# Performance work log

Measured on AMD Instinct MI355X. Metric: run time of the kernel, lower is better.

## Reference

```python
import jax, jax.numpy as jnp
import numpy as np

D, U, H = 3, 256, 8
DH = U // H
B, N, E = 128, 128, 512
BN_SCALE = 1.0 / np.sqrt(1.0 + 1e-3)  # keras BatchNorm inference with init moving stats (mean=0, var=1)


def setup_inputs() -> dict:
    key = jax.random.key(0)
    k = jax.random.split(key, 16)
    p = lambda kk, sh: jax.random.normal(kk, sh, jnp.float32) * 0.05
    return {
        "node_attr": jax.random.normal(k[0], (B, N, U), jnp.float32),
        "edge_attr": jax.random.normal(k[1], (B, E, U), jnp.float32),
        "edge_indices": jax.random.randint(k[2], (B, E, 2), 0, N, dtype=jnp.int32),
        "W_edge": p(k[3], (D, 3 * U, U)), "b_edge": jnp.zeros((D, U)),
        "gamma_e": jnp.ones((D, U)), "beta_e": jnp.zeros((D, U)),
        "W_node": p(k[4], (D, U, U)), "b_node": jnp.zeros((D, U)),
        "gamma_n": jnp.ones((D, U)), "beta_n": jnp.zeros((D, U)),
        "W_gat": p(k[5], (D, U, H, DH)), "a_gat": p(k[6], (D, H, 2 * DH + U)), "b_gat": jnp.zeros((D, H)),
        "W_gru": p(k[7], (D, U, 3 * U)), "U_gru": p(k[8], (D, U, 3 * U)), "b_gru": jnp.zeros((D, 3 * U)),
        "W_p1": p(k[9], (U, U)), "b_p1": jnp.zeros((U,)),
        "W_p2": p(k[10], (U, U // 2)), "b_p2": jnp.zeros((U // 2,)),
    }


def _bn(x, gamma, beta):
    # inference batchnorm with moving_mean=0, moving_var=1
    return x * (gamma * BN_SCALE) + beta


def _gather(nodes, idx):
    # nodes [B,N,F], idx [B,E] -> [B,E,F]
    return jnp.take_along_axis(nodes, idx[..., None], axis=1)


def _gat_one(h, eidx, edge, a, b):
    # h [N,H,DH], eidx [E,2], edge [E,U]; aggregate messages from src (col 1) at tgt (col 0)
    tgt, src = eidx[:, 0], eidx[:, 1]
    hi, hj = h[tgt], h[src]
    logit = (jnp.einsum('ehd,hd->eh', hi, a[:, :DH])
             + jnp.einsum('ehd,hd->eh', hj, a[:, DH:2 * DH])
             + edge @ a[:, 2 * DH:].T + b)
    logit = jax.nn.leaky_relu(logit, 0.2)
    # per-target-node segment softmax over variable-degree neighborhoods
    m = jnp.full((N, H), -1e9, logit.dtype).at[tgt].max(logit)
    ex = jnp.exp(logit - m[tgt])
    den = jnp.zeros((N, H), logit.dtype).at[tgt].add(ex) + 1e-9
    att = ex / den[tgt]
    out = jnp.zeros((N, H, DH), h.dtype).at[tgt].add(att[..., None] * hj)
    return out.reshape(N, H * DH)


def reference(node_attr, edge_attr, edge_indices, W_edge, b_edge, gamma_e, beta_e,
              W_node, b_node, gamma_n, beta_n, W_gat, a_gat, b_gat,
              W_gru, U_gru, b_gru, W_p1, b_p1, W_p2, b_p2):
    nodes, edges = node_attr, edge_attr
    tgt_idx = edge_indices[..., 0]
    src_idx = edge_indices[..., 1]
    for d in range(D):
        # edge update: gather endpoints, concat with edge feats, MLP, graph batchnorm
        e_in = _gather(nodes, src_idx)   # GatherNodesOutgoing
        e_out = _gather(nodes, tgt_idx)  # GatherNodesIngoing
        ec = jnp.concatenate([e_in, e_out, edges], axis=-1)  # [B,E,3U]
        e_up = _bn(jax.nn.relu(ec @ W_edge[d] + b_edge[d]), gamma_e[d], beta_e[d])
        # multi-head GAT attention over edges
        h = jnp.einsum('bnf,fhd->bnhd', nodes, W_gat[d])
        attended = jax.nn.relu(jax.vmap(_gat_one, in_axes=(0, 0, 0, None, None))(
            h, edge_indices, e_up, a_gat[d], b_gat[d]))
        # node MLP + batchnorm
        n_up = _bn(jax.nn.relu(nodes @ W_node[d] + b_node[d]), gamma_n[d], beta_n[d])
        # GRU update: state = n_up, input = attended
        xp = attended @ W_gru[d] + b_gru[d]
        hp = n_up @ U_gru[d]
        z = jax.nn.sigmoid(xp[..., :U] + hp[..., :U])
        r = jax.nn.sigmoid(xp[..., U:2 * U] + hp[..., U:2 * U])
        hh = jnp.tanh(xp[..., 2 * U:] + r * hp[..., 2 * U:])
        nodes = z * n_up + (1.0 - z) * hh
        edges = e_up
    emb = jnp.mean(nodes, axis=1)
    emb = jax.nn.relu(emb @ W_p1 + b_p1)
    emb = jax.nn.relu(emb @ W_p2 + b_p2)
    # inference-mode view augmentation is identity, so both views equal the base embedding
    views = jnp.stack([emb, emb], axis=1)  # [B, num_views, U//2]
    return emb, views
```

## Files before the change

### kernel.cpp

```cpp
#include <hip/hip_runtime.h>
#include <hip/hip_bf16.h>

constexpr int Dn  = 3;
constexpr int Un  = 256;
constexpr int Hn  = 8;
constexpr int DHn = 32;
constexpr int Bn  = 128;
constexpr int Nn  = 128;
constexpr int En  = 512;
constexpr float BN_SCALE_C = 0.9995003746877732f;

#define LB __launch_bounds__(256)
#define LB8 __launch_bounds__(512)

typedef short bf16x8 __attribute__((ext_vector_type(8)));
typedef unsigned short u16x8 __attribute__((ext_vector_type(8)));
typedef float f32x4 __attribute__((ext_vector_type(4)));
#define MFMA16(a, b, c) __builtin_amdgcn_mfma_f32_16x16x32_bf16(a, b, c, 0, 0, 0)

__device__ __forceinline__ void gload16(const void* g, void* l) {
  __builtin_amdgcn_global_load_lds(
      (const __attribute__((address_space(1))) void*)g,
      (__attribute__((address_space(3))) void*)l, 16, 0, 0);
}
__device__ __forceinline__ float sigm(float x) { return 1.f / (1.f + expf(-x)); }
__device__ __forceinline__ float bf2f(unsigned short u) {
  return __uint_as_float((unsigned)u << 16);
}

__global__ LB void k_f2bf(const float* __restrict__ in,
                          __hip_bfloat16* __restrict__ out, int n) {
  int i = (blockIdx.x * 256 + threadIdx.x) * 4;
  if (i + 3 < n) {
    float4 v = *reinterpret_cast<const float4*>(in + i);
    out[i + 0] = __float2bfloat16(v.x);
    out[i + 1] = __float2bfloat16(v.y);
    out[i + 2] = __float2bfloat16(v.z);
    out[i + 3] = __float2bfloat16(v.w);
  }
}

__global__ LB void k_prep_edge(const float* __restrict__ W,
                               __hip_bfloat16* __restrict__ Wt) {
  int idx = blockIdx.x * 256 + threadIdx.x;
  int d = idx / (Un * 3 * Un);
  int rem = idx % (Un * 3 * Un);
  int n = rem / (3 * Un);
  int k = rem % (3 * Un);
  Wt[idx] = __float2bfloat16(W[(size_t)d * 3 * Un * Un + (size_t)k * Un + n]);
}

__global__ LB void k_prep_hn(const float* __restrict__ Wg,
                             const float* __restrict__ Wn,
                             __hip_bfloat16* __restrict__ Wt) {
  int idx = blockIdx.x * 256 + threadIdx.x;
  int d = idx / (512 * 256);
  int rem = idx % (512 * 256);
  int n = rem / 256;
  int k = rem % 256;
  float v = (n < 256) ? Wg[(size_t)d * 65536 + k * 256 + n]
                      : Wn[(size_t)d * 65536 + k * 256 + (n - 256)];
  Wt[idx] = __float2bfloat16(v);
}

__global__ LB void k_prep_gru2(const float* __restrict__ W,
                               const float* __restrict__ U,
                               __hip_bfloat16* __restrict__ Wt) {
  int idx = blockIdx.x * 256 + threadIdx.x;
  int d = idx / (768 * 512);
  int rem = idx % (768 * 512);
  int j2 = rem >> 9;
  int k = rem & 511;
  const size_t wb = (size_t)d * 196608;
  float v = (k < 256) ? W[wb + k * 768 + j2] : U[wb + (k - 256) * 768 + j2];
  Wt[idx] = __float2bfloat16(v);
}

__global__ LB8 void k_edge_mfma(const __hip_bfloat16* __restrict__ nodes,
                                const __hip_bfloat16* __restrict__ edges,
                                const int* __restrict__ eidx,
                                const __hip_bfloat16* __restrict__ Wt,
                                const float* __restrict__ bias,
                                const float* __restrict__ gamma,
                                const float* __restrict__ beta,
                                __hip_bfloat16* __restrict__ e_up) {
  __shared__ __align__(16) short As[128 * 64];
  __shared__ __align__(16) short Bs[256 * 64];
  const int tid = threadIdx.x, lane = tid & 63;
  const int w = tid >> 6, wr = w >> 2, wc = w & 3;
  const int bid = blockIdx.x;
  const int wgid = (bid & 7) * 64 + (bid >> 3);
  const int row0 = wgid * 128;
  const __hip_bfloat16 *pa0[2], *pa1[2], *pa2[2], *pb[4];
  int sxa[2], sxb[4];
#pragma unroll
  for (int i = 0; i < 2; ++i) {
    int c = i * 512 + tid, row = c >> 3, slot = c & 7;
    int R = row0 + row, b = R >> 9, e = R & 511;
    int tt = eidx[(b * En + e) * 2 + 0];
    int ss = eidx[(b * En + e) * 2 + 1];
    pa0[i] = nodes + (size_t)(b * Nn + ss) * Un;
    pa1[i] = nodes + (size_t)(b * Nn + tt) * Un;
    pa2[i] = edges + (size_t)(b * En + e) * Un;
    sxa[i] = (slot ^ (row & 7)) * 8;
  }
#pragma unroll
  for (int i = 0; i < 4; ++i) {
    int c = i * 512 + tid, j = c >> 3, slot = c & 7;
    pb[i] = Wt + (size_t)j * 768;
    sxb[i] = (slot ^ (j & 7)) * 8;
  }
  f32x4 acc[4][4] = {};
  const int ldsb = (tid & 448) * 16;
  for (int kt = 0; kt < 768; kt += 64) {
    const int region = kt >> 8, koff = kt & 255;
#pragma unroll
    for (int i = 0; i < 2; ++i) {
      const __hip_bfloat16* s = (region == 0) ? pa0[i] : (region == 1 ? pa1[i] : pa2[i]);
      gload16(s + koff + sxa[i], (char*)As + i * 8192 + ldsb);
    }
#pragma unroll
    for (int i = 0; i < 4; ++i)
      gload16(pb[i] + kt + sxb[i], (char*)Bs + i * 8192 + ldsb);
    __syncthreads();
#pragma unroll
    for (int ks = 0; ks < 2; ++ks) {
      const int lc = ks * 4 + (lane >> 4);
      bf16x8 af[4], bfv[4];
#pragma unroll
      for (int mi = 0; mi < 4; ++mi) {
        int row = wr * 64 + mi * 16 + (lane & 15);
        af[mi] = *(const bf16x8*)((const char*)As + row * 128 + ((lc ^ (row & 7)) << 4));
      }
#pragma unroll
      for (int ni = 0; ni < 4; ++ni) {
        int col = wc * 64 + ni * 16 + (lane & 15);
        bfv[ni] = *(const bf16x8*)((const char*)Bs + col * 128 + ((lc ^ (col & 7)) << 4));
      }
#pragma unroll
      for (int mi = 0; mi < 4; ++mi)
#pragma unroll
        for (int ni = 0; ni < 4; ++ni)
          acc[mi][ni] = MFMA16(af[mi], bfv[ni], acc[mi][ni]);
    }
    __syncthreads();
  }
#pragma unroll
  for (int mi = 0; mi < 4; ++mi)
#pragma unroll
    for (int ni = 0; ni < 4; ++ni) {
      int C = wc * 64 + ni * 16 + (lane & 15);
      float gs = gamma[C] * BN_SCALE_C, bt = beta[C], bi = bias[C];
#pragma unroll
      for (int r = 0; r < 4; ++r) {
        int R = row0 + wr * 64 + mi * 16 + (lane >> 4) * 4 + r;
        float v = acc[mi][ni][r] + bi;
        v = fmaxf(v, 0.f) * gs + bt;
        e_up[(size_t)R * Un + C] = __float2bfloat16(v);
      }
    }
}

__global__ LB8 void k_hn_mfma(const __hip_bfloat16* __restrict__ A,
                              const __hip_bfloat16* __restrict__ Wt,
                              const float* __restrict__ nb,
                              const float* __restrict__ ng,
                              const float* __restrict__ nbe,
                              __hip_bfloat16* __restrict__ h_bf,
                              __hip_bfloat16* __restrict__ nupb) {
  __shared__ __align__(16) short As[128 * 64];
  __shared__ __align__(16) short Bs[256 * 64];
  const int tid = threadIdx.x, lane = tid & 63;
  const int w = tid >> 6, wr = w >> 2, wc = w & 3;
  const int bid = blockIdx.x;
  const int wgid = (bid & 7) * 32 + (bid >> 3);
  const int row0 = (wgid >> 1) * 128, col0 = (wgid & 1) * 256;
  const __hip_bfloat16 *pa[2], *pb[4];
  int sxa[2], sxb[4];
#pragma unroll
  for (int i = 0; i < 2; ++i) {
    int c = i * 512 + tid, row = c >> 3, slot = c & 7;
    pa[i] = A + (size_t)(row0 + row) * Un;
    sxa[i] = (slot ^ (row & 7)) * 8;
  }
#pragma unroll
  for (int i = 0; i < 4; ++i) {
    int c = i * 512 + tid, j = c >> 3, slot = c & 7;
    pb[i] = Wt + (size_t)(col0 + j) * Un;
    sxb[i] = (slot ^ (j & 7)) * 8;
  }
  f32x4 acc[4][4] = {};
  const int ldsb = (tid & 448) * 16;
  for (int kt = 0; kt < 256; kt += 64) {
#pragma unroll
    for (int i = 0; i < 2; ++i)
      gload16(pa[i] + kt + sxa[i], (char*)As + i * 8192 + ldsb);
#pragma unroll
    for (int i = 0; i < 4; ++i)
      gload16(pb[i] + kt + sxb[i], (char*)Bs + i * 8192 + ldsb);
    __syncthreads();
#pragma unroll
    for (int ks = 0; ks < 2; ++ks) {
      const int lc = ks * 4 + (lane >> 4);
      bf16x8 af[4], bfv[4];
#pragma unroll
      for (int mi = 0; mi < 4; ++mi) {
        int row = wr * 64 + mi * 16 + (lane & 15);
        af[mi] = *(const bf16x8*)((const char*)As + row * 128 + ((lc ^ (row & 7)) << 4));
      }
#pragma unroll
      for (int ni = 0; ni < 4; ++ni) {
        int col = wc * 64 + ni * 16 + (lane & 15);
        bfv[ni] = *(const bf16x8*)((const char*)Bs + col * 128 + ((lc ^ (col & 7)) << 4));
      }
#pragma unroll
      for (int mi = 0; mi < 4; ++mi)
#pragma unroll
        for (int ni = 0; ni < 4; ++ni)
          acc[mi][ni] = MFMA16(af[mi], bfv[ni], acc[mi][ni]);
    }
    __syncthreads();
  }
  const bool is_h = (col0 < 256);
#pragma unroll
  for (int mi = 0; mi < 4; ++mi)
#pragma unroll
    for (int ni = 0; ni < 4; ++ni) {
      int c2 = wc * 64 + ni * 16 + (lane & 15);
#pragma unroll
      for (int r = 0; r < 4; ++r) {
        int R = row0 + wr * 64 + mi * 16 + (lane >> 4) * 4 + r;
        float v = acc[mi][ni][r];
        if (is_h) {
          h_bf[(size_t)R * Un + c2] = __float2bfloat16(v);
        } else {
          v += nb[c2];
          v = fmaxf(v, 0.f) * (ng[c2] * BN_SCALE_C) + nbe[c2];
          nupb[(size_t)R * Un + c2] = __float2bfloat16(v);
        }
      }
    }
}

__global__ LB void k_gru_mfma2(const __hip_bfloat16* __restrict__ attb,
                               const __hip_bfloat16* __restrict__ nupb,
                               const __hip_bfloat16* __restrict__ Wt,
                               const float* __restrict__ bg,
                               __hip_bfloat16* __restrict__ nodes_out) {
  __shared__ __align__(16) short As[128 * 64];
  __shared__ __align__(16) short Bs[96 * 64];
  const int tid = threadIdx.x, lane = tid & 63;
  const int w = tid >> 6, wr = w >> 1, wc = w & 1;
  const int bid = blockIdx.x;
  const int wgid = (bid & 7) * 128 + (bid >> 3);
  const int row0 = (wgid >> 3) * 128, c0 = (wgid & 7) * 32;
  const __hip_bfloat16 *paA[4], *paN[4], *pb[3];
  int sxa[4], sxb[3];
#pragma unroll
  for (int i = 0; i < 4; ++i) {
    int c = i * 256 + tid, row = c >> 3, slot = c & 7;
    paA[i] = attb + (size_t)(row0 + row) * Un;
    paN[i] = nupb + (size_t)(row0 + row) * Un;
    sxa[i] = (slot ^ (row & 7)) * 8;
  }
#pragma unroll
  for (int i = 0; i < 3; ++i) {
    int l = i * 256 + tid, j = l >> 3, slot = l & 7;
    int grow = (j < 32) ? (c0 + j) : (j < 64) ? (256 + c0 + (j - 32))
                                              : (512 + c0 + (j - 64));
    pb[i] = Wt + (size_t)grow * 512;
    sxb[i] = (slot ^ (j & 7)) * 8;
  }
  f32x4 acc[4][4] = {};
  const int ldsb = (tid & 192) * 16;
  for (int kt = 0; kt < 512; kt += 64) {
    const int koff = kt & 255;
    const bool rA = kt < 256;
#pragma unroll
    for (int i = 0; i < 4; ++i) {
      const __hip_bfloat16* s = rA ? paA[i] : paN[i];
      gload16(s + koff + sxa[i], (char*)As + i * 4096 + ldsb);
    }
#pragma unroll
    for (int i = 0; i < 3; ++i)
      gload16(pb[i] + kt + sxb[i], (char*)Bs + i * 4096 + ldsb);
    __syncthreads();
    const int g2 = rA ? 2 : 3;
#pragma unroll
    for (int ks = 0; ks < 2; ++ks) {
      const int lc = ks * 4 + (lane >> 4);
      bf16x8 af[4], bv[3];
      const int jj = wc * 16 + (lane & 15);
      const int jsw = (lc ^ (jj & 7)) << 4;
      bv[0] = *(const bf16x8*)((const char*)Bs + jj * 128 + jsw);
      bv[1] = *(const bf16x8*)((const char*)Bs + (32 + jj) * 128 + jsw);
      bv[2] = *(const bf16x8*)((const char*)Bs + (64 + jj) * 128 + jsw);
#pragma unroll
      for (int mi = 0; mi < 4; ++mi) {
        int row = wr * 64 + mi * 16 + (lane & 15);
        af[mi] = *(const bf16x8*)((const char*)As + row * 128 + ((lc ^ (row & 7)) << 4));
      }
#pragma unroll
      for (int mi = 0; mi < 4; ++mi) {
        acc[0][mi] = MFMA16(af[mi], bv[0], acc[0][mi]);
        acc[1][mi] = MFMA16(af[mi], bv[1], acc[1][mi]);
        acc[g2][mi] = MFMA16(af[mi], bv[2], acc[g2][mi]);
      }
    }
    __syncthreads();
  }
  {
    const int c = c0 + wc * 16 + (lane & 15);
    const float bz = bg[c], br = bg[256 + c], bh = bg[512 + c];
    const unsigned short* nu_u = (const unsigned short*)nupb;
#pragma unroll
    for (int mi = 0; mi < 4; ++mi)
#pragma unroll
      for (int r = 0; r < 4; ++r) {
        int R = row0 + wr * 64 + mi * 16 + (lane >> 4) * 4 + r;
        float z  = sigm(acc[0][mi][r] + bz);
        float rr = sigm(acc[1][mi][r] + br);
        float hh = tanhf(acc[2][mi][r] + bh + rr * acc[3][mi][r]);
        float nu = bf2f(nu_u[(size_t)R * Un + c]);
        nodes_out[(size_t)R * Un + c] = __float2bfloat16(z * nu + (1.f - z) * hh);
      }
  }
}

__global__ LB void k_elog_mfma(const __hip_bfloat16* __restrict__ e_up,
                               const float* __restrict__ a_gat,
                               float* __restrict__ elog) {
  __shared__ __align__(16) short at[16 * 264];
  const int tid = threadIdx.x, lane = tid & 63, w = tid >> 6;
  for (int l = tid; l < 16 * 264; l += 256) {
    int col = l / 264, k = l % 264;
    float v = (col < 8 && k < 256) ? a_gat[col * 320 + 64 + k] : 0.f;
    __hip_bfloat16 b = __float2bfloat16(v);
    at[l] = *reinterpret_cast<short*>(&b);
  }
  __syncthreads();
  const int rowbase = blockIdx.x * 256 + w * 64;
  const int lrow = lane & 15, lk = (lane >> 4) * 8;
  f32x4 acc[4] = {};
#pragma unroll
  for (int kt = 0; kt < 256; kt += 32) {
    bf16x8 bf = *(const bf16x8*)(at + lrow * 264 + kt + lk);
#pragma unroll
    for (int mi = 0; mi < 4; ++mi) {
      bf16x8 af = *(const bf16x8*)(e_up + (size_t)(rowbase + mi * 16 + lrow) * 256 + kt + lk);
      acc[mi] = MFMA16(af, bf, acc[mi]);
    }
  }
  if (lrow < 8) {
#pragma unroll
    for (int mi = 0; mi < 4; ++mi)
#pragma unroll
      for (int r = 0; r < 4; ++r) {
        int row = rowbase + mi * 16 + (lane >> 4) * 4 + r;
        elog[(size_t)row * 8 + lrow] = acc[mi][r];
      }
  }
}

__global__ LB void k_gat3(const __hip_bfloat16* __restrict__ h,
                          const float* __restrict__ elog,
                          const int* __restrict__ eidx,
                          const float* __restrict__ a_gat,
                          const float* __restrict__ b_gat,
                          __hip_bfloat16* __restrict__ att_bf) {
  const int b = blockIdx.x, hg = blockIdx.y;
  __shared__ int s_tgt[En], s_src[En];
  __shared__ float s_at[4][32], s_as[4][32];
  __shared__ float s_lt[Nn][4], s_ls[Nn][4];
  __shared__ float s_L[En][4];
  __shared__ int s_cnt[Nn], s_start[Nn], s_cur[Nn];
  __shared__ short s_ord[En];
  __shared__ float s_bg[4];
  __shared__ __align__(16) unsigned short hl[Nn][136];
  const int tid = threadIdx.x;
  if (tid < 4) s_bg[tid] = b_gat[hg * 4 + tid];
  if (tid < 128) {
    int q = tid >> 5, d = tid & 31;
    s_at[q][d] = a_gat[(hg * 4 + q) * 320 + d];
    s_as[q][d] = a_gat[(hg * 4 + q) * 320 + 32 + d];
  }
  for (int e = tid; e < En; e += 256) {
    s_tgt[e] = eidx[(b * En + e) * 2 + 0];
    s_src[e] = eidx[(b * En + e) * 2 + 1];
  }
  for (int l = tid; l < Nn; l += 256) s_cnt[l] = 0;
  for (int l = tid; l < En * 4; l += 256) {
    int e = l >> 2, q = l & 3;
    s_L[e][q] = elog[(size_t)(b * En + e) * 8 + hg * 4 + q];
  }
  const unsigned short* hu = (const unsigned short*)h;
  for (int l = tid; l < Nn * 16; l += 256) {
    int row = l >> 4, c8 = l & 15;
    u16x8 v = *(const u16x8*)(hu + (size_t)(b * Nn + row) * Un + hg * 128 + c8 * 8);
    *(u16x8*)&hl[row][c8 * 8] = v;
  }
  __syncthreads();
  for (int p = tid; p < Nn * 4; p += 256) {
    int n = p >> 2, q = p & 3;
    const unsigned short* hr = &hl[n][q * 32];
    float lt = 0.f, ls = 0.f;
#pragma unroll
    for (int c8 = 0; c8 < 4; ++c8) {
      u16x8 v = *(const u16x8*)(hr + c8 * 8);
#pragma unroll
      for (int j = 0; j < 8; ++j) {
        float f = bf2f(v[j]);
        int d = c8 * 8 + j;
        lt += f * s_at[q][d];
        ls += f * s_as[q][d];
      }
    }
    s_lt[n][q] = lt; s_ls[n][q] = ls;
  }
  for (int e = tid; e < En; e += 256) atomicAdd(&s_cnt[s_tgt[e]], 1);
  __syncthreads();
  if (tid == 0) {
    int acc = 0;
    for (int n = 0; n < Nn; ++n) { s_start[n] = acc; s_cur[n] = acc; acc += s_cnt[n]; }
  }
  __syncthreads();
  for (int e = tid; e < En; e += 256) {
    int pos = atomicAdd(&s_cur[s_tgt[e]], 1);
    s_ord[pos] = (short)e;
  }
  for (int l = tid; l < En * 4; l += 256) {
    int e = l >> 2, q = l & 3;
    float v = s_lt[s_tgt[e]][q] + s_ls[s_src[e]][q] + s_L[e][q] + s_bg[q];
    v = (v > 0.f) ? v : 0.2f * v;
    s_L[e][q] = v;
  }
  __syncthreads();
  for (int p = tid; p < Nn * 4; p += 256) {
    const int n = p >> 2, q = p & 3;
    const int st = s_start[n], cn = s_cnt[n];
    float m = -1e9f;
    for (int i = 0; i < cn; ++i) m = fmaxf(m, s_L[s_ord[st + i]][q]);
    float den = 1e-9f;
    for (int i = 0; i < cn; ++i) {
      const int e = s_ord[st + i];
      float ex = expf(s_L[e][q] - m);
      s_L[e][q] = ex;
      den += ex;
    }
    const float inv = 1.f / den;
    float acc[32] = {};
    for (int i = 0; i < cn; ++i) {
      const int e = s_ord[st + i];
      const float wgt = s_L[e][q] * inv;
      const unsigned short* hs = &hl[s_src[e]][q * 32];
#pragma unroll
      for (int c8 = 0; c8 < 4; ++c8) {
        u16x8 v = *(const u16x8*)(hs + c8 * 8);
#pragma unroll
        for (int j = 0; j < 8; ++j) acc[c8 * 8 + j] += wgt * bf2f(v[j]);
      }
    }
    __hip_bfloat16* ob = att_bf + (size_t)(b * Nn + n) * Un + (hg * 4 + q) * DHn;
#pragma unroll
    for (int d = 0; d < 32; ++d) ob[d] = __float2bfloat16(fmaxf(acc[d], 0.f));
  }
}

__global__ LB void k_pool(const __hip_bfloat16* __restrict__ nodes,
                          const float* __restrict__ Wp1, const float* __restrict__ bp1,
                          const float* __restrict__ Wp2, const float* __restrict__ bp2,
                          float* __restrict__ out) {
  const int b = blockIdx.x, tid = threadIdx.x;
  __shared__ float e0[256], e1[256];
  float s = 0.f;
  for (int n = 0; n < Nn; ++n) s += __bfloat162float(nodes[(size_t)(b * Nn + n) * Un + tid]);
  e0[tid] = s * (1.f / Nn);
  __syncthreads();
  float a1 = bp1[tid];
  for (int k = 0; k < 256; ++k) a1 += e0[k] * Wp1[k * 256 + tid];
  e1[tid] = fmaxf(a1, 0.f);
  __syncthreads();
  if (tid < 128) {
    float a2 = bp2[tid];
    for (int k = 0; k < 256; ++k) a2 += e1[k] * Wp2[k * 128 + tid];
    a2 = fmaxf(a2, 0.f);
    out[b * 128 + tid] = a2;
    out[Bn * 128 + b * 256 + tid] = a2;
    out[Bn * 128 + b * 256 + 128 + tid] = a2;
  }
}

extern "C" void kernel_launch(void* const* d_in, const int* in_sizes, int n_in,
                              void* d_out, int out_size, void* d_ws, size_t ws_size,
                              hipStream_t stream) {
  const float* node_attr = (const float*)d_in[0];
  const float* edge_attr = (const float*)d_in[1];
  const int*   eidx      = (const int*)d_in[2];
  const float* W_edge    = (const float*)d_in[3];
  const float* b_edge    = (const float*)d_in[4];
  const float* gamma_e   = (const float*)d_in[5];
  const float* beta_e    = (const float*)d_in[6];
  const float* W_node    = (const float*)d_in[7];
  const float* b_node    = (const float*)d_in[8];
  const float* gamma_n   = (const float*)d_in[9];
  const float* beta_n    = (const float*)d_in[10];
  const float* W_gat     = (const float*)d_in[11];
  const float* a_gat     = (const float*)d_in[12];
  const float* b_gat     = (const float*)d_in[13];
  const float* W_gru     = (const float*)d_in[14];
  const float* U_gru     = (const float*)d_in[15];
  const float* b_gru     = (const float*)d_in[16];
  const float* W_p1      = (const float*)d_in[17];
  const float* b_p1      = (const float*)d_in[18];
  const float* W_p2      = (const float*)d_in[19];
  const float* b_p2      = (const float*)d_in[20];

  char* p = (char*)d_ws;
  auto alloc = [&](size_t bytes) { char* q = p; p += (bytes + 255) & ~255ull; return q; };
  const size_t NODE_EL = (size_t)Bn * Nn * Un;
  const size_t EDGE_EL = (size_t)Bn * En * Un;
  __hip_bfloat16* nodes_bf = (__hip_bfloat16*)alloc(NODE_EL * 2);
  __hip_bfloat16* h_bf   = (__hip_bfloat16*)alloc(NODE_EL * 2);
  __hip_bfloat16* nup_bf = (__hip_bfloat16*)alloc(NODE_EL * 2);
  __hip_bfloat16* att_bf = (__hip_bfloat16*)alloc(NODE_EL * 2);
  float* elog   = (float*)alloc((size_t)Bn * En * 8 * 4);
  __hip_bfloat16* edges_a = (__hip_bfloat16*)alloc(EDGE_EL * 2);
  __hip_bfloat16* edges_b = (__hip_bfloat16*)alloc(EDGE_EL * 2);
  __hip_bfloat16* Wt_e   = (__hip_bfloat16*)alloc((size_t)Dn * 256 * 768 * 2);
  __hip_bfloat16* Wt_hn  = (__hip_bfloat16*)alloc((size_t)Dn * 512 * 256 * 2);
  __hip_bfloat16* Wt_gru = (__hip_bfloat16*)alloc((size_t)Dn * 768 * 512 * 2);

  k_f2bf<<<(int)(EDGE_EL / 1024), 256, 0, stream>>>(edge_attr, edges_a, (int)EDGE_EL);
  k_f2bf<<<(int)(NODE_EL / 1024), 256, 0, stream>>>(node_attr, nodes_bf, (int)NODE_EL);
  k_prep_edge<<<(Dn * 256 * 768) / 256, 256, 0, stream>>>(W_edge, Wt_e);
  k_prep_hn<<<(Dn * 512 * 256) / 256, 256, 0, stream>>>(W_gat, W_node, Wt_hn);
  k_prep_gru2<<<(Dn * 768 * 512) / 256, 256, 0, stream>>>(W_gru, U_gru, Wt_gru);

  __hip_bfloat16* ein = edges_a;
  __hip_bfloat16* eout = edges_b;
  for (int d = 0; d < Dn; ++d) {
    k_edge_mfma<<<512, 512, 0, stream>>>(
        nodes_bf, ein, eidx, Wt_e + (size_t)d * 256 * 768, b_edge + d * Un,
        gamma_e + d * Un, beta_e + d * Un, eout);
    k_hn_mfma<<<256, 512, 0, stream>>>(
        nodes_bf, Wt_hn + (size_t)d * 512 * 256, b_node + d * Un,
        gamma_n + d * Un, beta_n + d * Un, h_bf, nup_bf);
    k_elog_mfma<<<(Bn * En) / 256, 256, 0, stream>>>(
        eout, a_gat + (size_t)d * Hn * 320, elog);
    k_gat3<<<dim3(Bn, 2), 256, 0, stream>>>(
        h_bf, elog, eidx, a_gat + (size_t)d * Hn * 320, b_gat + d * Hn, att_bf);
    k_gru_mfma2<<<1024, 256, 0, stream>>>(
        att_bf, nup_bf, Wt_gru + (size_t)d * 768 * 512, b_gru + d * 3 * Un,
        nodes_bf);
    __hip_bfloat16* t = ein; ein = eout; eout = t;
  }
  k_pool<<<Bn, 256, 0, stream>>>(nodes_bf, W_p1, b_p1, W_p2, b_p2, (float*)d_out);
}
```

Before: 369.4 us.

## Split GAT kernel per head and widen GRU GEMM tile to 512 threads

The GAT aggregation kernel now launches one block per (batch, head) instead of per (batch, 4-head group), giving 4x more blocks. It also splits the weighted-sum accumulation across two threads per node, using 16 accumulators each instead of 32. The GRU GEMM moves to 512-thread blocks covering 64 output columns per gate instead of 32, halving the grid and reusing each A tile across more columns. The trade-off is more redundant index/count setup per GAT block and higher per-block LDS and register pressure in the GRU kernel.

```diff
diff --git a/kernel.cpp b/kernel.cpp
--- a/kernel.cpp
+++ b/kernel.cpp
@@ -242,59 +242,58 @@
     }
 }
 
-__global__ LB void k_gru_mfma2(const __hip_bfloat16* __restrict__ attb,
-                               const __hip_bfloat16* __restrict__ nupb,
-                               const __hip_bfloat16* __restrict__ Wt,
-                               const float* __restrict__ bg,
-                               __hip_bfloat16* __restrict__ nodes_out) {
+__global__ LB8 void k_gru_mfma3(const __hip_bfloat16* __restrict__ attb,
+                                const __hip_bfloat16* __restrict__ nupb,
+                                const __hip_bfloat16* __restrict__ Wt,
+                                const float* __restrict__ bg,
+                                __hip_bfloat16* __restrict__ nodes_out) {
   __shared__ __align__(16) short As[128 * 64];
-  __shared__ __align__(16) short Bs[96 * 64];
+  __shared__ __align__(16) short Bs[192 * 64];
   const int tid = threadIdx.x, lane = tid & 63;
-  const int w = tid >> 6, wr = w >> 1, wc = w & 1;
+  const int w = tid >> 6, wr = w >> 2, wc = w & 3;
   const int bid = blockIdx.x;
-  const int wgid = (bid & 7) * 128 + (bid >> 3);
-  const int row0 = (wgid >> 3) * 128, c0 = (wgid & 7) * 32;
-  const __hip_bfloat16 *paA[4], *paN[4], *pb[3];
-  int sxa[4], sxb[3];
-#pragma unroll
-  for (int i = 0; i < 4; ++i) {
-    int c = i * 256 + tid, row = c >> 3, slot = c & 7;
+  const int wgid = (bid & 7) * 64 + (bid >> 3);
+  const int row0 = (wgid >> 2) * 128, c0 = (wgid & 3) * 64;
+  const __hip_bfloat16 *paA[2], *paN[2], *pb[3];
+  int sxa[2], sxb[3];
+#pragma unroll
+  for (int i = 0; i < 2; ++i) {
+    int c = i * 512 + tid, row = c >> 3, slot = c & 7;
     paA[i] = attb + (size_t)(row0 + row) * Un;
     paN[i] = nupb + (size_t)(row0 + row) * Un;
     sxa[i] = (slot ^ (row & 7)) * 8;
   }
 #pragma unroll
   for (int i = 0; i < 3; ++i) {
-    int l = i * 256 + tid, j = l >> 3, slot = l & 7;
-    int grow = (j < 32) ? (c0 + j) : (j < 64) ? (256 + c0 + (j - 32))
-                                              : (512 + c0 + (j - 64));
-    pb[i] = Wt + (size_t)grow * 512;
+    int l = i * 512 + tid, j = l >> 3, slot = l & 7;
+    int sec = j >> 6, jj = j & 63;
+    pb[i] = Wt + (size_t)(sec * 256 + c0 + jj) * 512;
     sxb[i] = (slot ^ (j & 7)) * 8;
   }
   f32x4 acc[4][4] = {};
-  const int ldsb = (tid & 192) * 16;
+  const int ldsb = (tid & 448) * 16;
   for (int kt = 0; kt < 512; kt += 64) {
     const int koff = kt & 255;
     const bool rA = kt < 256;
 #pragma unroll
-    for (int i = 0; i < 4; ++i) {
+    for (int i = 0; i < 2; ++i) {
       const __hip_bfloat16* s = rA ? paA[i] : paN[i];
-      gload16(s + koff + sxa[i], (char*)As + i * 4096 + ldsb);
+      gload16(s + koff + sxa[i], (char*)As + i * 8192 + ldsb);
     }
 #pragma unroll
     for (int i = 0; i < 3; ++i)
-      gload16(pb[i] + kt + sxb[i], (char*)Bs + i * 4096 + ldsb);
+      gload16(pb[i] + kt + sxb[i], (char*)Bs + i * 8192 + ldsb);
     __syncthreads();
     const int g2 = rA ? 2 : 3;
 #pragma unroll
     for (int ks = 0; ks < 2; ++ks) {
       const int lc = ks * 4 + (lane >> 4);
       bf16x8 af[4], bv[3];
-      const int jj = wc * 16 + (lane & 15);
-      const int jsw = (lc ^ (jj & 7)) << 4;
-      bv[0] = *(const bf16x8*)((const char*)Bs + jj * 128 + jsw);
-      bv[1] = *(const bf16x8*)((const char*)Bs + (32 + jj) * 128 + jsw);
-      bv[2] = *(const bf16x8*)((const char*)Bs + (64 + jj) * 128 + jsw);
+#pragma unroll
+      for (int s = 0; s < 3; ++s) {
+        int j = s * 64 + wc * 16 + (lane & 15);
+        bv[s] = *(const bf16x8*)((const char*)Bs + j * 128 + ((lc ^ (j & 7)) << 4));
+      }
 #pragma unroll
       for (int mi = 0; mi < 4; ++mi) {
         int row = wr * 64 + mi * 16 + (lane & 15);
@@ -362,47 +361,42 @@
   }
 }
 
-__global__ LB void k_gat3(const __hip_bfloat16* __restrict__ h,
+__global__ LB void k_gat4(const __hip_bfloat16* __restrict__ h,
                           const float* __restrict__ elog,
                           const int* __restrict__ eidx,
                           const float* __restrict__ a_gat,
                           const float* __restrict__ b_gat,
                           __hip_bfloat16* __restrict__ att_bf) {
-  const int b = blockIdx.x, hg = blockIdx.y;
+  const int b = blockIdx.x, q = blockIdx.y;
   __shared__ int s_tgt[En], s_src[En];
-  __shared__ float s_at[4][32], s_as[4][32];
-  __shared__ float s_lt[Nn][4], s_ls[Nn][4];
-  __shared__ float s_L[En][4];
+  __shared__ float s_at[32], s_as[32];
+  __shared__ float s_lt[Nn], s_ls[Nn];
+  __shared__ float s_L[En];
   __shared__ int s_cnt[Nn], s_start[Nn], s_cur[Nn];
   __shared__ short s_ord[En];
-  __shared__ float s_bg[4];
-  __shared__ __align__(16) unsigned short hl[Nn][136];
+  __shared__ __align__(16) unsigned short hl[Nn][40];
   const int tid = threadIdx.x;
-  if (tid < 4) s_bg[tid] = b_gat[hg * 4 + tid];
-  if (tid < 128) {
-    int q = tid >> 5, d = tid & 31;
-    s_at[q][d] = a_gat[(hg * 4 + q) * 320 + d];
-    s_as[q][d] = a_gat[(hg * 4 + q) * 320 + 32 + d];
+  const float bgq = b_gat[q];
+  if (tid < 32) {
+    s_at[tid] = a_gat[q * 320 + tid];
+    s_as[tid] = a_gat[q * 320 + 32 + tid];
   }
   for (int e = tid; e < En; e += 256) {
     s_tgt[e] = eidx[(b * En + e) * 2 + 0];
     s_src[e] = eidx[(b * En + e) * 2 + 1];
   }
-  for (int l = tid; l < Nn; l += 256) s_cnt[l] = 0;
-  for (int l = tid; l < En * 4; l += 256) {
-    int e = l >> 2, q = l & 3;
-    s_L[e][q] = elog[(size_t)(b * En + e) * 8 + hg * 4 + q];
-  }
+  if (tid < Nn) s_cnt[tid] = 0;
+  for (int e = tid; e < En; e += 256)
+    s_L[e] = elog[(size_t)(b * En + e) * 8 + q];
   const unsigned short* hu = (const unsigned short*)h;
-  for (int l = tid; l < Nn * 16; l += 256) {
-    int row = l >> 4, c8 = l & 15;
-    u16x8 v = *(const u16x8*)(hu + (size_t)(b * Nn + row) * Un + hg * 128 + c8 * 8);
+  for (int l = tid; l < Nn * 4; l += 256) {
+    int row = l >> 2, c8 = l & 3;
+    u16x8 v = *(const u16x8*)(hu + (size_t)(b * Nn + row) * Un + q * DHn + c8 * 8);
     *(u16x8*)&hl[row][c8 * 8] = v;
   }
   __syncthreads();
-  for (int p = tid; p < Nn * 4; p += 256) {
-    int n = p >> 2, q = p & 3;
-    const unsigned short* hr = &hl[n][q * 32];
+  if (tid < Nn) {
+    const unsigned short* hr = hl[tid];
     float lt = 0.f, ls = 0.f;
 #pragma unroll
     for (int c8 = 0; c8 < 4; ++c8) {
@@ -411,11 +405,11 @@
       for (int j = 0; j < 8; ++j) {
         float f = bf2f(v[j]);
         int d = c8 * 8 + j;
-        lt += f * s_at[q][d];
-        ls += f * s_as[q][d];
-      }
-    }
-    s_lt[n][q] = lt; s_ls[n][q] = ls;
+        lt += f * s_at[d];
+        ls += f * s_as[d];
+      }
+    }
+    s_lt[tid] = lt; s_ls[tid] = ls;
   }
   for (int e = tid; e < En; e += 256) atomicAdd(&s_cnt[s_tgt[e]], 1);
   __syncthreads();
@@ -428,41 +422,45 @@
     int pos = atomicAdd(&s_cur[s_tgt[e]], 1);
     s_ord[pos] = (short)e;
   }
-  for (int l = tid; l < En * 4; l += 256) {
-    int e = l >> 2, q = l & 3;
-    float v = s_lt[s_tgt[e]][q] + s_ls[s_src[e]][q] + s_L[e][q] + s_bg[q];
+  for (int e = tid; e < En; e += 256) {
+    float v = s_lt[s_tgt[e]] + s_ls[s_src[e]] + s_L[e] + bgq;
     v = (v > 0.f) ? v : 0.2f * v;
-    s_L[e][q] = v;
-  }
-  __syncthreads();
-  for (int p = tid; p < Nn * 4; p += 256) {
-    const int n = p >> 2, q = p & 3;
-    const int st = s_start[n], cn = s_cnt[n];
+    s_L[e] = v;
+  }
+  __syncthreads();
+  if (tid < Nn) {
+    const int st = s_start[tid], cn = s_cnt[tid];
     float m = -1e9f;
-    for (int i = 0; i < cn; ++i) m = fmaxf(m, s_L[s_ord[st + i]][q]);
+    for (int i = 0; i < cn; ++i) m = fmaxf(m, s_L[s_ord[st + i]]);
     float den = 1e-9f;
     for (int i = 0; i < cn; ++i) {
       const int e = s_ord[st + i];
-      float ex = expf(s_L[e][q] - m);
-      s_L[e][q] = ex;
+      float ex = expf(s_L[e] - m);
+      s_L[e] = ex;
       den += ex;
     }
-    const float inv = 1.f / den;
-    float acc[32] = {};
+    s_lt[tid] = 1.f / den;
+  }
+  __syncthreads();
+  {
+    const int n = tid >> 1, half = tid & 1;
+    const int st = s_start[n], cn = s_cnt[n];
+    const float inv = s_lt[n];
+    float acc[16] = {};
     for (int i = 0; i < cn; ++i) {
       const int e = s_ord[st + i];
-      const float wgt = s_L[e][q] * inv;
-      const unsigned short* hs = &hl[s_src[e]][q * 32];
-#pragma unroll
-      for (int c8 = 0; c8 < 4; ++c8) {
+      const float wgt = s_L[e] * inv;
+      const unsigned short* hs = &hl[s_src[e]][half * 16];
+#pragma unroll
+      for (int c8 = 0; c8 < 2; ++c8) {
         u16x8 v = *(const u16x8*)(hs + c8 * 8);
 #pragma unroll
         for (int j = 0; j < 8; ++j) acc[c8 * 8 + j] += wgt * bf2f(v[j]);
       }
     }
-    __hip_bfloat16* ob = att_bf + (size_t)(b * Nn + n) * Un + (hg * 4 + q) * DHn;
-#pragma unroll
-    for (int d = 0; d < 32; ++d) ob[d] = __float2bfloat16(fmaxf(acc[d], 0.f));
+    __hip_bfloat16* ob = att_bf + (size_t)(b * Nn + n) * Un + q * DHn + half * 16;
+#pragma unroll
+    for (int d = 0; d < 16; ++d) ob[d] = __float2bfloat16(fmaxf(acc[d], 0.f));
   }
 }
 
@@ -547,9 +545,9 @@
         gamma_n + d * Un, beta_n + d * Un, h_bf, nup_bf);
     k_elog_mfma<<<(Bn * En) / 256, 256, 0, stream>>>(
         eout, a_gat + (size_t)d * Hn * 320, elog);
-    k_gat3<<<dim3(Bn, 2), 256, 0, stream>>>(
+    k_gat4<<<dim3(Bn, Hn), 256, 0, stream>>>(
         h_bf, elog, eidx, a_gat + (size_t)d * Hn * 320, b_gat + d * Hn, att_bf);
-    k_gru_mfma2<<<1024, 256, 0, stream>>>(
+    k_gru_mfma3<<<512, 512, 0, stream>>>(
         att_bf, nup_bf, Wt_gru + (size_t)d * 768 * 512, b_gru + d * 3 * Un,
         nodes_bf);
     __hip_bfloat16* t = ein; ein = eout; eout = t;
```

Measured after the change: 366.6 us, median of 2. No clear change (-0.8%).
